# Optimization experiments

Hardware: AMD Instinct MI355X
Metric: run time of the kernel (lower is better)

The kernel has to match this reference:

```python
import jax, jax.numpy as jnp
import numpy as np

B, V, S = 128, 64, 40
D, H, VOC = 256, 256, 20000


def setup_inputs() -> dict:
    key = jax.random.key(0)
    ks = jax.random.split(key, 26)
    g = lambda k, shp: (jax.random.normal(k, shp, dtype=jnp.float32) * 0.02)
    inp = {}
    inp['input_seqs'] = jax.random.randint(ks[0], (B, V, S), 0, VOC + 1)
    inp['mask'] = jnp.zeros((B, V), jnp.float32)
    inp['length'] = jax.random.randint(ks[1], (B,), 1, V + 1)
    inp['seq_time_step'] = jax.random.uniform(ks[2], (B, V), dtype=jnp.float32)
    inp['codemask'] = jnp.zeros((B, V, S), jnp.float32)
    inp['label'] = jax.random.randint(ks[3], (B,), 0, 2)
    # embedding table; padding_idx=-1 in torch == row VOC zeroed
    inp['emb'] = g(ks[4], (VOC + 1, D)).at[VOC].set(0.0)
    # LSTM (single layer, batch_first): torch gate order i,f,g,o
    inp['W_ih'] = g(ks[5], (4 * H, D))
    inp['W_hh'] = g(ks[6], (4 * H, H))
    inp['b_ih'] = g(ks[7], (4 * H,))
    inp['b_hh'] = g(ks[8], (4 * H,))
    # attention projections
    inp['Whk'] = g(ks[9], (D, H))
    inp['bhk'] = g(ks[10], (D,))
    inp['W1'] = g(ks[11], (64, 2 * H))
    inp['b1'] = g(ks[12], (64,))
    inp['W2'] = g(ks[13], (2, 64))
    inp['b2'] = g(ks[14], (2,))
    # classifyer MLP: d -> 4d -> 2d -> 2
    inp['C1W'] = g(ks[15], (4 * D, D))
    inp['C1b'] = g(ks[16], (4 * D,))
    inp['C2W'] = g(ks[17], (2 * D, 4 * D))
    inp['C2b'] = g(ks[18], (2 * D,))
    inp['CoW'] = g(ks[19], (2, 2 * D))
    inp['Cob'] = g(ks[20], (2,))
    return inp


def _lstm(x, W_ih, W_hh, b_ih, b_hh):
    # x: [B,T,D] -> hs: [B,T,H]; torch gate order i,f,g,o
    Bsz = x.shape[0]
    Hd = W_hh.shape[1]
    xg = jnp.einsum('btd,gd->btg', x, W_ih) + b_ih + b_hh  # [B,T,4H]

    def step(carry, xg_t):
        h, c = carry
        gates = xg_t + h @ W_hh.T
        i, f, gg, o = jnp.split(gates, 4, axis=-1)
        i = jax.nn.sigmoid(i); f = jax.nn.sigmoid(f)
        gg = jnp.tanh(gg); o = jax.nn.sigmoid(o)
        c = f * c + i * gg
        h = o * jnp.tanh(c)
        return (h, c), h

    z = jnp.zeros((Bsz, Hd), x.dtype)
    _, hs = jax.lax.scan(step, (z, z), jnp.swapaxes(xg, 0, 1))
    return jnp.swapaxes(hs, 0, 1)


def _classify(h, C1W, C1b, C2W, C2b, CoW, Cob):
    h = jax.nn.relu(h @ C1W.T + C1b)
    h = jax.nn.relu(h @ C2W.T + C2b)
    return h @ CoW.T + Cob


def reference(input_seqs, mask, length, seq_time_step, codemask, label,
              emb, W_ih, W_hh, b_ih, b_hh, Whk, bhk, W1, b1, W2, b2,
              C1W, C1b, C2W, C2b, CoW, Cob):
    # before(): embedding gather -> relu -> sum over codes (eval mode, no dropout)
    v = jax.nn.relu(emb[input_seqs]).sum(-2)  # [B,V,D]
    h = _lstm(v, W_ih, W_hh, b_ih, b_hh)       # [B,V,H]

    # vectorized form of the per-timestep attention loop:
    # bar_v[:,0]=v[:,0]; for i>=1: mix of e_k=v[:,0] and w_hk(h[:,i-1])
    e_k = v[:, :1, :]                                   # [B,1,D]
    wh = h @ Whk.T + bhk                                # [B,V,D]
    wh_prev = wh[:, :-1, :]                             # [B,V-1,D] (h at i-1)
    e_b = jnp.broadcast_to(e_k, wh_prev.shape)
    cat = jnp.concatenate([e_b, wh_prev], axis=-1)      # [B,V-1,2D]
    attn = jax.nn.softmax(jnp.tanh(cat @ W1.T + b1) @ W2.T + b2, axis=-1)
    bar_rest = e_b * attn[..., 0:1] + wh_prev * attn[..., 1:2]
    bar_v = jnp.concatenate([v[:, :1, :], bar_rest], axis=1)  # [B,V,D]

    # GAN stand-in (external injected module): identity
    Dec_V, Gen_V = bar_v, bar_v
    gen_h = _lstm(Gen_V, W_ih, W_hh, b_ih, b_hh)

    og = _classify(h, C1W, C1b, C2W, C2b, CoW, Cob)        # [B,V,2]
    fake = _classify(gen_h, C1W, C1b, C2W, C2b, CoW, Cob)  # [B,V,2]
    final_og = og[:, -1, :]
    final_fake = fake[:, -1, :]
    return (final_og, final_fake, Dec_V, Gen_V, seq_time_step, label)
```

## Files before the change

### kernel.cpp

```cpp
#include <hip/hip_runtime.h>

#define DEV __device__ __forceinline__

typedef float f32x4 __attribute__((ext_vector_type(4)));
typedef short s16x8 __attribute__((ext_vector_type(8)));
typedef short s16x4 __attribute__((ext_vector_type(4)));

DEV unsigned short f2bf(float f){
  unsigned int u = __float_as_uint(f);
  u += 0x7fffu + ((u>>16)&1u);
  return (unsigned short)(u>>16);
}
DEV float bf2f(unsigned short h){ return __uint_as_float(((unsigned int)h)<<16); }

#if __has_builtin(__builtin_amdgcn_rcpf)
DEV float frcp_(float x){ return __builtin_amdgcn_rcpf(x); }
#else
DEV float frcp_(float x){ return 1.f/x; }
#endif
#if __has_builtin(__builtin_amdgcn_exp2f)
DEV float fexp2_(float x){ return __builtin_amdgcn_exp2f(x); }
#else
DEV float fexp2_(float x){ return exp2f(x); }
#endif

DEV float sigm(float x){ return frcp_(1.f + fexp2_(-1.4426950408889634f*x)); }
DEV float tanh_(float x){
  x = fminf(x, 30.f);
  float e = fexp2_(2.8853900817779268f*x);
  return (e-1.f)*frcp_(e+1.f);
}

DEV unsigned char f2e4m3(float x){
  unsigned int u = __float_as_uint(x);
  unsigned int s = (u>>24)&0x80u;
  unsigned int mag = u & 0x7fffffffu;
  if (mag > 0x43E00000u) mag = 0x43E00000u;
  mag += 0x000FFFFFu + ((mag>>20)&1u);
  int e = (int)(mag>>23) - 120;
  unsigned int m = (mag>>20)&7u;
  unsigned int r = (e<=0) ? 0u : (((unsigned)e<<3)|m);
  return (unsigned char)(s|r);
}

DEV f32x4 mfma_bf16(s16x8 a, s16x8 b, f32x4 c){
  return __builtin_amdgcn_mfma_f32_16x16x32_bf16(a,b,c,0,0,0);
}
DEV f32x4 mfma_fp8(long a, long b, f32x4 c){
  return __builtin_amdgcn_mfma_f32_16x16x32_fp8_fp8(a,b,c,0,0,0);
}

DEV void lds_barrier(){
  asm volatile("s_waitcnt lgkmcnt(0)\n\ts_barrier" ::: "memory");
}

#define Bx 128
#define Vx 64
#define Sx 40
#define Dx 256
#define Hx 256

#define OFF_OG   0
#define OFF_FAKE 256
#define OFF_DECV 512
#define OFF_GENV 2097664
#define OFF_STS  4194816
#define OFF_LBL  4203008

#define PW_IH  0
#define PW_HH  262144
#define PW_HK  524288
#define PW_1   589824
#define PC_1   622592
#define PC_2   884736
#define PC_O   1409024
#define P_TOT  1410048

__global__ void k_cvtall(const float* __restrict__ W_ih, const float* __restrict__ Whh,
                         const float* __restrict__ Whk, const float* __restrict__ W1,
                         const float* __restrict__ C1W, const float* __restrict__ C2W,
                         const float* __restrict__ CoW, unsigned short* __restrict__ dst,
                         unsigned char* __restrict__ dst8){
  int i = blockIdx.x*256 + threadIdx.x;
  if (i < P_TOT){
    float v;
    if      (i < PW_HH) v = W_ih[i - PW_IH];
    else if (i < PW_HK) v = Whh [i - PW_HH];
    else if (i < PW_1 ) v = Whk [i - PW_HK];
    else if (i < PC_1 ) v = W1  [i - PW_1 ];
    else if (i < PC_2 ) v = C1W [i - PC_1 ];
    else if (i < PC_O ) v = C2W [i - PC_2 ];
    else                v = CoW [i - PC_O ];
    dst[i] = f2bf(v);
  } else if (i < P_TOT + 262144){
    dst8[i - P_TOT] = f2e4m3(16.f*Whh[i - P_TOT]);
  }
}

__global__ void k_embed(const int* __restrict__ seqs, const float* __restrict__ emb,
                        float* __restrict__ v32, unsigned short* __restrict__ v16,
                        float* __restrict__ decv, float* __restrict__ genv,
                        unsigned short* __restrict__ barv16){
  int bt = blockIdx.x;
  int d = threadIdx.x;
  const int* sp = seqs + (size_t)bt*Sx;
  float acc = 0.f;
  #pragma unroll 4
  for (int s=0;s<Sx;s++){
    int id = sp[s];
    acc += fmaxf(emb[(size_t)id*Dx + d], 0.f);
  }
  size_t o = (size_t)bt*Dx + d;
  v32[o] = acc;
  v16[o] = f2bf(acc);
  if ((bt & 63) == 0){
    decv[o] = acc; genv[o] = acc; barv16[o] = f2bf(acc);
  }
}

template<int MODE_A, int MODE_C, int RELU>
__global__ void k_gemm(const unsigned short* __restrict__ A, const unsigned short* __restrict__ Bw,
                       const float* __restrict__ bias1, const float* __restrict__ bias2,
                       unsigned short* __restrict__ C, int K, int Ntot, float scale){
  int tid = threadIdx.x, w = tid>>6, l = tid&63, lm = l&15, q = l>>4;
  int m0 = blockIdx.x*64;
  int n0 = blockIdx.y*256 + w*64;
  f32x4 acc[4][4];
  #pragma unroll
  for (int nt=0;nt<4;nt++){
    int n = n0 + nt*16 + lm;
    float bz = bias1 ? bias1[n] : 0.f;
    if (bias2) bz += bias2[n];
    #pragma unroll
    for (int mt=0;mt<4;mt++) acc[mt][nt] = (f32x4){bz,bz,bz,bz};
  }
  const s16x8* Arow[4];
  #pragma unroll
  for (int mt=0;mt<4;mt++){
    int m = m0 + mt*16 + lm;
    size_t off = (MODE_A==0) ? (size_t)m*K : ((size_t)(m&127)*Vx + (m>>7))*(size_t)K;
    Arow[mt] = (const s16x8*)(A + off);
  }
  int kkn = K/32;
  for (int kk=0; kk<kkn; kk++){
    s16x8 bfr[4];
    #pragma unroll
    for (int nt=0;nt<4;nt++){
      int n = n0 + nt*16 + lm;
      bfr[nt] = *(const s16x8*)(Bw + (size_t)n*K + kk*32 + q*8);
    }
    #pragma unroll
    for (int mt=0;mt<4;mt++){
      s16x8 afr = Arow[mt][kk*4 + q];
      #pragma unroll
      for (int nt=0;nt<4;nt++)
        acc[mt][nt] = mfma_bf16(afr, bfr[nt], acc[mt][nt]);
    }
  }
  #pragma unroll
  for (int mt=0;mt<4;mt++){
    int mbase = m0 + mt*16 + q*4;
    #pragma unroll
    for (int nt=0;nt<4;nt++){
      int n = n0 + nt*16 + lm;
      if (MODE_C==0){
        #pragma unroll
        for (int r=0;r<4;r++){
          float val = scale*acc[mt][nt][r];
          if (RELU) val = fmaxf(val, 0.f);
          C[(size_t)(mbase+r)*Ntot + n] = f2bf(val);
        }
      } else {
        int tt = mbase>>7, bb = mbase&127;
        int gg = bb>>4, b4 = bb&15;
        s16x4 sv;
        #pragma unroll
        for (int r=0;r<4;r++){
          float val = scale*acc[mt][nt][r];
          if (RELU) val = fmaxf(val, 0.f);
          sv[r] = (short)f2bf(val);
        }
        *(s16x4*)(C + (((size_t)tt*8 + gg)*1024 + n)*16 + b4) = sv;
      }
    }
  }
}

#define HPB 264
template<int STORE_ALL>
__global__ __launch_bounds__(1024) void k_scan(const unsigned char* __restrict__ W8,
        const unsigned short* __restrict__ xg, unsigned short* __restrict__ hist){
  __shared__ __align__(16) unsigned char hl[2][16*HPB];
  int tid = threadIdx.x;
  int g = blockIdx.x;
  int w = tid>>6, l = tid&63, lm = l&15, q = l>>4;
  int j = w*16 + lm;
  for (int i=tid;i<2*16*HPB;i+=1024) ((unsigned char*)hl)[i] = 0;
  long Bf[4][8];
  #pragma unroll
  for (int qq=0;qq<4;qq++){
    int n = qq*256 + j;
    #pragma unroll
    for (int kk=0;kk<8;kk++)
      Bf[qq][kk] = *(const long*)(W8 + (size_t)n*256 + kk*32 + q*8);
  }
  float cst[4] = {0.f,0.f,0.f,0.f};
  const unsigned short* xgb = xg + (size_t)g*16384 + q*4;
  s16x4 xc[4], xn[4];
  #pragma unroll
  for (int qq=0;qq<4;qq++) xc[qq] = *(const s16x4*)(xgb + (qq*256+j)*16);
  __syncthreads();
  const float K1 = 1.4426950408889634f/256.f;
  #pragma unroll 1
  for (int t=0;t<Vx;t++){
    if (t < Vx-1){
      #pragma unroll
      for (int qq=0;qq<4;qq++)
        xn[qq] = *(const s16x4*)(xgb + (size_t)(t+1)*131072 + (qq*256+j)*16);
    }
    f32x4 acc[4];
    #pragma unroll
    for (int qq=0;qq<4;qq++){
      #pragma unroll
      for (int r=0;r<4;r++) acc[qq][r] = bf2f((unsigned short)xc[qq][r]);
    }
    const unsigned char* hb = hl[t&1];
    #pragma unroll
    for (int kk=0;kk<8;kk++){
      long af = *(const long*)(hb + lm*HPB + kk*32 + q*8);
      acc[0] = mfma_fp8(af, Bf[0][kk], acc[0]);
      acc[1] = mfma_fp8(af, Bf[1][kk], acc[1]);
      acc[2] = mfma_fp8(af, Bf[2][kk], acc[2]);
      acc[3] = mfma_fp8(af, Bf[3][kk], acc[3]);
    }
    unsigned char* hn = hl[(t+1)&1];
    float hv16[4];
    #pragma unroll
    for (int r=0;r<4;r++){
      float iv = frcp_(1.f + fexp2_(-K1*acc[0][r]));
      float fv = frcp_(1.f + fexp2_(-K1*acc[1][r]));
      float eg = fexp2_(2.f*K1*acc[2][r]);
      float gv = (eg-1.f)*frcp_(eg+1.f);
      float ov = frcp_(1.f + fexp2_(-K1*acc[3][r]));
      float cv = fv*cst[r] + iv*gv;
      cst[r] = cv;
      float ec = fexp2_(2.8853900817779268f*fminf(cv,30.f));
      float hv = ov*(ec-1.f)*frcp_(ec+1.f);
      hv16[r] = 16.f*hv;
      if (STORE_ALL)
        hist[((size_t)t*Bx + g*16 + q*4 + r)*Hx + j] = f2bf(hv);
      else if (t==Vx-1)
        hist[((size_t)(g*16 + q*4 + r))*Hx + j] = f2bf(hv);
    }
#if __has_builtin(__builtin_amdgcn_cvt_pk_fp8_f32)
    int p01 = __builtin_amdgcn_cvt_pk_fp8_f32(hv16[0], hv16[1], 0, false);
    int p23 = __builtin_amdgcn_cvt_pk_fp8_f32(hv16[2], hv16[3], 0, false);
    hn[(q*4+0)*HPB + j] = (unsigned char)p01;
    hn[(q*4+1)*HPB + j] = (unsigned char)(p01>>8);
    hn[(q*4+2)*HPB + j] = (unsigned char)p23;
    hn[(q*4+3)*HPB + j] = (unsigned char)(p23>>8);
#else
    #pragma unroll
    for (int r=0;r<4;r++) hn[(q*4+r)*HPB + j] = f2e4m3(hv16[r]);
#endif
    #pragma unroll
    for (int qq=0;qq<4;qq++) xc[qq] = xn[qq];
    lds_barrier();
  }
}

__global__ void k_u(const float* __restrict__ v32, const float* __restrict__ W1,
                    const float* __restrict__ b1, float* __restrict__ u){
  int b = blockIdx.x, n = threadIdx.x;
  const f32x4* vr = (const f32x4*)(v32 + (size_t)b*Vx*Dx);
  const f32x4* wr = (const f32x4*)(W1 + (size_t)n*512);
  float a = b1[n];
  for (int kk=0;kk<64;kk++){
    f32x4 x = vr[kk], ww = wr[kk];
    a += x[0]*ww[0] + x[1]*ww[1] + x[2]*ww[2] + x[3]*ww[3];
  }
  u[(size_t)b*64 + n] = a;
}

__global__ void k_attn(const unsigned short* __restrict__ wh16,
                       const float* __restrict__ v32, const float* __restrict__ u,
                       const unsigned short* __restrict__ W116, const float* __restrict__ W2,
                       const float* __restrict__ b2,
                       float* __restrict__ decv, float* __restrict__ genv,
                       unsigned short* __restrict__ barv16){
  int tid = threadIdx.x, w = tid>>6, l = tid&63, lm = l&15, q = l>>4;
  int mt = blockIdx.x*4 + w;
  int m0 = mt*16;
  f32x4 acc[4];
  #pragma unroll
  for (int nt=0;nt<4;nt++){
    int n = nt*16 + lm;
    f32x4 a;
    #pragma unroll
    for (int r=0;r<4;r++) a[r] = u[(size_t)((m0 + q*4 + r)&127)*64 + n];
    acc[nt] = a;
  }
  const s16x8* Arow = (const s16x8*)(wh16 + (size_t)(m0+lm)*Dx);
  #pragma unroll
  for (int kk=0;kk<8;kk++){
    s16x8 af = Arow[kk*4 + q];
    #pragma unroll
    for (int nt=0;nt<4;nt++){
      int n = nt*16 + lm;
      s16x8 bf = *(const s16x8*)(W116 + (size_t)n*512 + 256 + kk*32 + q*8);
      acc[nt] = mfma_bf16(af, bf, acc[nt]);
    }
  }
  float p0a[4] = {0,0,0,0}, p1a[4] = {0,0,0,0};
  #pragma unroll
  for (int nt=0;nt<4;nt++){
    int n = nt*16 + lm;
    float w2a = W2[n], w2b = W2[64+n];
    #pragma unroll
    for (int r=0;r<4;r++){
      float z = tanh_(acc[nt][r]);
      p0a[r] += z*w2a; p1a[r] += z*w2b;
    }
  }
  #pragma unroll
  for (int s=1;s<16;s<<=1){
    #pragma unroll
    for (int r=0;r<4;r++){ p0a[r] += __shfl_xor(p0a[r], s, 16); p1a[r] += __shfl_xor(p1a[r], s, 16); }
  }
  float bb0 = b2[0], bb1 = b2[1];
  int t = m0>>7;
  int d0 = lm*16;
  #pragma unroll
  for (int r=0;r<4;r++){
    int m = m0 + q*4 + r; int b = m&127;
    float a0 = p0a[r]+bb0, a1 = p1a[r]+bb1;
    float al0 = frcp_(1.f + fexp2_(1.4426950408889634f*(a1-a0)));
    float al1 = 1.f - al0;
    const f32x4* ek = (const f32x4*)(v32 + (size_t)b*Vx*Dx + d0);
    const unsigned short* whr = wh16 + (size_t)m*Dx + d0;
    size_t ob = ((size_t)b*Vx + (t+1))*Dx + d0;
    #pragma unroll
    for (int c=0;c<4;c++){
      f32x4 e = ek[c], o;
      s16x4 o16;
      #pragma unroll
      for (int jj=0;jj<4;jj++){
        o[jj] = al0*e[jj] + al1*bf2f(whr[c*4+jj]);
        o16[jj] = (short)f2bf(o[jj]);
      }
      *(f32x4*)(decv + ob + c*4) = o;
      *(f32x4*)(genv + ob + c*4) = o;
      *(s16x4*)(barv16 + ob + c*4) = o16;
    }
  }
}

__global__ void k_out(const unsigned short* __restrict__ y2, const unsigned short* __restrict__ CoW16,
                      const float* __restrict__ Cob, float* __restrict__ out){
  int tid = blockIdx.x*256 + threadIdx.x;
  int m = tid>>1, n = tid&1;
  const s16x8* yr = (const s16x8*)(y2 + (size_t)m*512);
  const s16x8* wr = (const s16x8*)(CoW16 + (size_t)n*512);
  float a = Cob[n];
  for (int kk=0;kk<64;kk++){
    s16x8 yv = yr[kk], ww = wr[kk];
    #pragma unroll
    for (int jj=0;jj<8;jj++) a += bf2f((unsigned short)yv[jj])*bf2f((unsigned short)ww[jj]);
  }
  int base = (m < 128) ? (OFF_OG + m*2) : (OFF_FAKE + (m-128)*2);
  out[base + n] = a;
}

__global__ void k_copy(const float* __restrict__ sts, const int* __restrict__ label,
                       float* __restrict__ out){
  int i = blockIdx.x*256 + threadIdx.x;
  if (i < Bx*Vx) out[OFF_STS + i] = sts[i];
  if (i < Bx)    out[OFF_LBL + i] = (float)label[i];
}

extern "C" void kernel_launch(void* const* d_in, const int* in_sizes, int n_in,
                              void* d_out, int out_size, void* d_ws, size_t ws_size,
                              hipStream_t stream) {
  const int*   seqs  = (const int*)d_in[0];
  const float* sts   = (const float*)d_in[3];
  const int*   label = (const int*)d_in[5];
  const float* emb   = (const float*)d_in[6];
  const float* W_ih  = (const float*)d_in[7];
  const float* W_hh  = (const float*)d_in[8];
  const float* b_ih  = (const float*)d_in[9];
  const float* b_hh  = (const float*)d_in[10];
  const float* Whk   = (const float*)d_in[11];
  const float* bhk   = (const float*)d_in[12];
  const float* W1    = (const float*)d_in[13];
  const float* b1    = (const float*)d_in[14];
  const float* W2    = (const float*)d_in[15];
  const float* b2    = (const float*)d_in[16];
  const float* C1b   = (const float*)d_in[18];
  const float* C2b   = (const float*)d_in[20];
  const float* Cob   = (const float*)d_in[22];
  float* out = (float*)d_out;

  char* ws = (char*)d_ws;
  unsigned short* v16    = (unsigned short*)(ws + 0);
  unsigned short* xg     = (unsigned short*)(ws + (4<<20));
  unsigned short* hist1  = (unsigned short*)(ws + (20<<20));
  unsigned short* wh16   = (unsigned short*)(ws + (25<<20));
  unsigned short* barv16 = (unsigned short*)(ws + (29<<20));
  float*          v32    = (float*)(ws + (33<<20));
  float*          u      = (float*)(ws + (41<<20));
  unsigned char*  whh8   = (unsigned char*)(ws + (41<<20) + (512<<10));
  unsigned short* pool   = (unsigned short*)(ws + (42<<20));
  unsigned short* y1     = (unsigned short*)(ws + (45<<20));
  unsigned short* y2     = (unsigned short*)(ws + (45<<20) + (512<<10));

  unsigned short* h2 = hist1 + (size_t)Vx*Bx*Hx;
  unsigned short* X  = hist1 + (size_t)(Vx-1)*Bx*Hx;

  float* decv = out + OFF_DECV;
  float* genv = out + OFF_GENV;

  k_cvtall<<<dim3(6532), dim3(256), 0, stream>>>(W_ih, W_hh, Whk, W1,
      (const float*)d_in[17], (const float*)d_in[19], (const float*)d_in[21], pool, whh8);
  k_embed<<<dim3(Bx*Vx), dim3(256), 0, stream>>>(seqs, emb, v32, v16, decv, genv, barv16);
  k_gemm<1,1,0><<<dim3(128,4), dim3(256), 0, stream>>>(v16, pool+PW_IH, b_ih, b_hh, xg, 256, 1024, 256.f);
  k_scan<1><<<dim3(8), dim3(1024), 0, stream>>>(whh8, xg, hist1);
  k_u<<<dim3(128), dim3(64), 0, stream>>>(v32, W1, b1, u);
  k_gemm<0,0,0><<<dim3(128,1), dim3(256), 0, stream>>>(hist1, pool+PW_HK, bhk, nullptr, wh16, 256, 256, 1.f);
  k_attn<<<dim3(126), dim3(256), 0, stream>>>(wh16, v32, u, pool+PW_1, W2, b2, decv, genv, barv16);
  k_gemm<1,1,0><<<dim3(128,4), dim3(256), 0, stream>>>(barv16, pool+PW_IH, b_ih, b_hh, xg, 256, 1024, 256.f);
  k_scan<0><<<dim3(8), dim3(1024), 0, stream>>>(whh8, xg, h2);
  k_gemm<0,0,1><<<dim3(4,4), dim3(256), 0, stream>>>(X, pool+PC_1, C1b, nullptr, y1, 256, 1024, 1.f);
  k_gemm<0,0,1><<<dim3(4,2), dim3(256), 0, stream>>>(y1, pool+PC_2, C2b, nullptr, y2, 1024, 512, 1.f);
  k_out<<<dim3(2), dim3(256), 0, stream>>>(y2, pool+PC_O, Cob, out);
  k_copy<<<dim3(32), dim3(256), 0, stream>>>(sts, label, out);
}
```

Baseline: 595.3 us.

## Fold k_u and copy into scan blocks, interleave gate MFMAs with activations

The first LSTM scan launch gets 9 extra blocks that compute the attention u-projection and copy seq_time_step/label, which removes two small kernel launches and lets that work overlap the scan's idle CUs. Inside the scan loop, the four gate MFMA chains now run one after another, each followed by its activation math, so transcendental work can overlap the next gate's matrix ops. Odd waves get raised priority with s_setprio. The cost is higher register pressure and a more complex kernel signature.

```diff
diff --git a/kernel.cpp b/kernel.cpp
--- a/kernel.cpp
+++ b/kernel.cpp
@@ -189,13 +189,37 @@
 #define HPB 264
 template<int STORE_ALL>
 __global__ __launch_bounds__(1024) void k_scan(const unsigned char* __restrict__ W8,
-        const unsigned short* __restrict__ xg, unsigned short* __restrict__ hist){
+        const unsigned short* __restrict__ xg, unsigned short* __restrict__ hist,
+        const float* __restrict__ v32, const float* __restrict__ W1,
+        const float* __restrict__ b1, float* __restrict__ u,
+        const float* __restrict__ sts, const int* __restrict__ label,
+        float* __restrict__ out){
+  int tid = threadIdx.x;
+  if (STORE_ALL && blockIdx.x >= 8){
+    int bid = blockIdx.x - 8;
+    if (bid < 8){
+      int t2 = bid*1024 + tid;
+      int b = t2>>6, n = t2&63;
+      const f32x4* vr = (const f32x4*)(v32 + (size_t)b*Vx*Dx);
+      const f32x4* wr = (const f32x4*)(W1 + (size_t)n*512);
+      float a = b1[n];
+      for (int kk=0;kk<64;kk++){
+        f32x4 x = vr[kk], ww = wr[kk];
+        a += x[0]*ww[0] + x[1]*ww[1] + x[2]*ww[2] + x[3]*ww[3];
+      }
+      u[(size_t)b*64 + n] = a;
+    } else {
+      for (int i=tid;i<Bx*Vx;i+=1024) out[OFF_STS + i] = sts[i];
+      if (tid < Bx) out[OFF_LBL + tid] = (float)label[tid];
+    }
+    return;
+  }
   __shared__ __align__(16) unsigned char hl[2][16*HPB];
-  int tid = threadIdx.x;
   int g = blockIdx.x;
   int w = tid>>6, l = tid&63, lm = l&15, q = l>>4;
   int j = w*16 + lm;
   for (int i=tid;i<2*16*HPB;i+=1024) ((unsigned char*)hl)[i] = 0;
+  if (w & 1) asm volatile("s_setprio 1");
   long Bf[4][8];
   #pragma unroll
   for (int qq=0;qq<4;qq++){
@@ -211,6 +235,7 @@
   for (int qq=0;qq<4;qq++) xc[qq] = *(const s16x4*)(xgb + (qq*256+j)*16);
   __syncthreads();
   const float K1 = 1.4426950408889634f/256.f;
+  const unsigned char* hrd = hl[0] + lm*HPB + q*8;
   #pragma unroll 1
   for (int t=0;t<Vx;t++){
     if (t < Vx-1){
@@ -218,31 +243,46 @@
       for (int qq=0;qq<4;qq++)
         xn[qq] = *(const s16x4*)(xgb + (size_t)(t+1)*131072 + (qq*256+j)*16);
     }
-    f32x4 acc[4];
-    #pragma unroll
-    for (int qq=0;qq<4;qq++){
-      #pragma unroll
-      for (int r=0;r<4;r++) acc[qq][r] = bf2f((unsigned short)xc[qq][r]);
-    }
-    const unsigned char* hb = hl[t&1];
-    #pragma unroll
-    for (int kk=0;kk<8;kk++){
-      long af = *(const long*)(hb + lm*HPB + kk*32 + q*8);
-      acc[0] = mfma_fp8(af, Bf[0][kk], acc[0]);
-      acc[1] = mfma_fp8(af, Bf[1][kk], acc[1]);
-      acc[2] = mfma_fp8(af, Bf[2][kk], acc[2]);
-      acc[3] = mfma_fp8(af, Bf[3][kk], acc[3]);
-    }
-    unsigned char* hn = hl[(t+1)&1];
+    const unsigned char* hb = hrd + (t&1)*(16*HPB);
+    f32x4 a0;
+    #pragma unroll
+    for (int r=0;r<4;r++) a0[r] = bf2f((unsigned short)xc[0][r]);
+    #pragma unroll
+    for (int kk=0;kk<8;kk++) a0 = mfma_fp8(*(const long*)(hb + kk*32), Bf[0][kk], a0);
+    float iv[4];
+    #pragma unroll
+    for (int r=0;r<4;r++) iv[r] = frcp_(1.f + fexp2_(-K1*a0[r]));
+    f32x4 a1;
+    #pragma unroll
+    for (int r=0;r<4;r++) a1[r] = bf2f((unsigned short)xc[1][r]);
+    #pragma unroll
+    for (int kk=0;kk<8;kk++) a1 = mfma_fp8(*(const long*)(hb + kk*32), Bf[1][kk], a1);
+    float fv[4];
+    #pragma unroll
+    for (int r=0;r<4;r++) fv[r] = frcp_(1.f + fexp2_(-K1*a1[r]));
+    f32x4 a2;
+    #pragma unroll
+    for (int r=0;r<4;r++) a2[r] = bf2f((unsigned short)xc[2][r]);
+    #pragma unroll
+    for (int kk=0;kk<8;kk++) a2 = mfma_fp8(*(const long*)(hb + kk*32), Bf[2][kk], a2);
+    float cvn[4];
+    #pragma unroll
+    for (int r=0;r<4;r++){
+      float eg = fexp2_(2.f*K1*a2[r]);
+      float gv = (eg-1.f)*frcp_(eg+1.f);
+      cvn[r] = fv[r]*cst[r] + iv[r]*gv;
+    }
+    f32x4 a3;
+    #pragma unroll
+    for (int r=0;r<4;r++) a3[r] = bf2f((unsigned short)xc[3][r]);
+    #pragma unroll
+    for (int kk=0;kk<8;kk++) a3 = mfma_fp8(*(const long*)(hb + kk*32), Bf[3][kk], a3);
+    unsigned char* hn = hl[(t+1)&1] + j;
     float hv16[4];
     #pragma unroll
     for (int r=0;r<4;r++){
-      float iv = frcp_(1.f + fexp2_(-K1*acc[0][r]));
-      float fv = frcp_(1.f + fexp2_(-K1*acc[1][r]));
-      float eg = fexp2_(2.f*K1*acc[2][r]);
-      float gv = (eg-1.f)*frcp_(eg+1.f);
-      float ov = frcp_(1.f + fexp2_(-K1*acc[3][r]));
-      float cv = fv*cst[r] + iv*gv;
+      float ov = frcp_(1.f + fexp2_(-K1*a3[r]));
+      float cv = cvn[r];
       cst[r] = cv;
       float ec = fexp2_(2.8853900817779268f*fminf(cv,30.f));
       float hv = ov*(ec-1.f)*frcp_(ec+1.f);
@@ -255,31 +295,18 @@
 #if __has_builtin(__builtin_amdgcn_cvt_pk_fp8_f32)
     int p01 = __builtin_amdgcn_cvt_pk_fp8_f32(hv16[0], hv16[1], 0, false);
     int p23 = __builtin_amdgcn_cvt_pk_fp8_f32(hv16[2], hv16[3], 0, false);
-    hn[(q*4+0)*HPB + j] = (unsigned char)p01;
-    hn[(q*4+1)*HPB + j] = (unsigned char)(p01>>8);
-    hn[(q*4+2)*HPB + j] = (unsigned char)p23;
-    hn[(q*4+3)*HPB + j] = (unsigned char)(p23>>8);
+    hn[(q*4+0)*HPB] = (unsigned char)p01;
+    hn[(q*4+1)*HPB] = (unsigned char)(p01>>8);
+    hn[(q*4+2)*HPB] = (unsigned char)p23;
+    hn[(q*4+3)*HPB] = (unsigned char)(p23>>8);
 #else
     #pragma unroll
-    for (int r=0;r<4;r++) hn[(q*4+r)*HPB + j] = f2e4m3(hv16[r]);
+    for (int r=0;r<4;r++) hn[(q*4+r)*HPB] = f2e4m3(hv16[r]);
 #endif
     #pragma unroll
     for (int qq=0;qq<4;qq++) xc[qq] = xn[qq];
     lds_barrier();
   }
-}
-
-__global__ void k_u(const float* __restrict__ v32, const float* __restrict__ W1,
-                    const float* __restrict__ b1, float* __restrict__ u){
-  int b = blockIdx.x, n = threadIdx.x;
-  const f32x4* vr = (const f32x4*)(v32 + (size_t)b*Vx*Dx);
-  const f32x4* wr = (const f32x4*)(W1 + (size_t)n*512);
-  float a = b1[n];
-  for (int kk=0;kk<64;kk++){
-    f32x4 x = vr[kk], ww = wr[kk];
-    a += x[0]*ww[0] + x[1]*ww[1] + x[2]*ww[2] + x[3]*ww[3];
-  }
-  u[(size_t)b*64 + n] = a;
 }
 
 __global__ void k_attn(const unsigned short* __restrict__ wh16,
@@ -369,13 +396,6 @@
   }
   int base = (m < 128) ? (OFF_OG + m*2) : (OFF_FAKE + (m-128)*2);
   out[base + n] = a;
-}
-
-__global__ void k_copy(const float* __restrict__ sts, const int* __restrict__ label,
-                       float* __restrict__ out){
-  int i = blockIdx.x*256 + threadIdx.x;
-  if (i < Bx*Vx) out[OFF_STS + i] = sts[i];
-  if (i < Bx)    out[OFF_LBL + i] = (float)label[i];
 }
 
 extern "C" void kernel_launch(void* const* d_in, const int* in_sizes, int n_in,
@@ -423,14 +443,14 @@
       (const float*)d_in[17], (const float*)d_in[19], (const float*)d_in[21], pool, whh8);
   k_embed<<<dim3(Bx*Vx), dim3(256), 0, stream>>>(seqs, emb, v32, v16, decv, genv, barv16);
   k_gemm<1,1,0><<<dim3(128,4), dim3(256), 0, stream>>>(v16, pool+PW_IH, b_ih, b_hh, xg, 256, 1024, 256.f);
-  k_scan<1><<<dim3(8), dim3(1024), 0, stream>>>(whh8, xg, hist1);
-  k_u<<<dim3(128), dim3(64), 0, stream>>>(v32, W1, b1, u);
+  k_scan<1><<<dim3(17), dim3(1024), 0, stream>>>(whh8, xg, hist1,
+      v32, W1, b1, u, sts, label, out);
   k_gemm<0,0,0><<<dim3(128,1), dim3(256), 0, stream>>>(hist1, pool+PW_HK, bhk, nullptr, wh16, 256, 256, 1.f);
   k_attn<<<dim3(126), dim3(256), 0, stream>>>(wh16, v32, u, pool+PW_1, W2, b2, decv, genv, barv16);
   k_gemm<1,1,0><<<dim3(128,4), dim3(256), 0, stream>>>(barv16, pool+PW_IH, b_ih, b_hh, xg, 256, 1024, 256.f);
-  k_scan<0><<<dim3(8), dim3(1024), 0, stream>>>(whh8, xg, h2);
+  k_scan<0><<<dim3(8), dim3(1024), 0, stream>>>(whh8, xg, h2,
+      nullptr, nullptr, nullptr, nullptr, nullptr, nullptr, nullptr);
   k_gemm<0,0,1><<<dim3(4,4), dim3(256), 0, stream>>>(X, pool+PC_1, C1b, nullptr, y1, 256, 1024, 1.f);
   k_gemm<0,0,1><<<dim3(4,2), dim3(256), 0, stream>>>(y1, pool+PC_2, C2b, nullptr, y2, 1024, 512, 1.f);
   k_out<<<dim3(2), dim3(256), 0, stream>>>(y2, pool+PC_O, Cob, out);
-  k_copy<<<dim3(32), dim3(256), 0, stream>>>(sts, label, out);
-}
+}
```

Measured after the change: 597.0 us. About the same (+0.3%).
